# Kernel tuning notes

Hardware: AMD Instinct MI355X
Metric: run time of the kernel (lower is better)

## Reference

```python
import jax, jax.numpy as jnp
import numpy as np

DIM = 128; D_STATE = 16; D_CONV = 4; EXPAND = 2
D_INNER = DIM * EXPAND            # 256
DT_RANK = (DIM + 15) // 16        # 8
B, H, W = 2, 56, 56


def _ln(x, w, b):
    m = jnp.mean(x, -1, keepdims=True)
    v = jnp.var(x, -1, keepdims=True)
    return (x - m) * jax.lax.rsqrt(v + 1e-5) * w + b


def _mamba(x, in_w, conv_w, conv_b, xproj_w, dt_w, dt_b, A_log, Dp, out_w):
    # x: (B, L, DIM)
    Bb, L, _ = x.shape
    xz = x @ in_w.T                                   # (B,L,2*D_INNER)
    xi, z = jnp.split(xz, 2, axis=-1)
    # causal depthwise conv1d (pad left d_conv-1, truncate to L)
    xc = jnp.transpose(xi, (0, 2, 1))                 # (B,D_INNER,L)
    xc = jax.lax.conv_general_dilated(
        xc, conv_w, (1,), [(D_CONV - 1, 0)],
        dimension_numbers=('NCH', 'OIH', 'NCH'),
        feature_group_count=D_INNER) + conv_b[None, :, None]
    xs = jax.nn.silu(jnp.transpose(xc, (0, 2, 1)))    # (B,L,D_INNER)
    dbl = xs @ xproj_w.T                              # (B,L,DT_RANK+2*D_STATE)
    dt = jax.nn.softplus(dbl[..., :DT_RANK] @ dt_w.T + dt_b)   # (B,L,D_INNER)
    Bc = dbl[..., DT_RANK:DT_RANK + D_STATE]          # (B,L,D_STATE)
    Cc = dbl[..., DT_RANK + D_STATE:]                 # (B,L,D_STATE)
    A = -jnp.exp(A_log)                               # (D_INNER,D_STATE)
    dA = jnp.exp(dt[..., None] * A)                   # (B,L,D_INNER,D_STATE)
    dBu = (dt * xs)[..., None] * Bc[:, :, None, :]    # (B,L,D_INNER,D_STATE)

    def step(h, inp):
        a, bu, c = inp
        h = a * h + bu                                # (B,D_INNER,D_STATE)
        return h, jnp.einsum('bdn,bn->bd', h, c)

    h0 = jnp.zeros((Bb, D_INNER, D_STATE), x.dtype)
    _, ys = jax.lax.scan(step, h0, (jnp.moveaxis(dA, 1, 0),
                                    jnp.moveaxis(dBu, 1, 0),
                                    jnp.moveaxis(Cc, 1, 0)))
    y = jnp.moveaxis(ys, 0, 1) + xs * Dp              # (B,L,D_INNER)
    y = y * jax.nn.silu(z)
    return y @ out_w.T                                # (B,L,DIM)


def _forward(x, norm_h_w, norm_h_b, norm_v_w, norm_v_b,
             dw_w, dw_b, pw_w, pw_b,
             h_in_w, h_conv_w, h_conv_b, h_xproj_w, h_dt_w, h_dt_b, h_A_log, h_D, h_out_w,
             v_in_w, v_conv_w, v_conv_b, v_xproj_w, v_dt_w, v_dt_b, v_A_log, v_D, v_out_w,
             ca_fc1_w, ca_fc2_w):
    Bb, C, Hh, Ww = x.shape
    # local branch: depthwise 3x3 + GELU + 1x1
    lf = jax.lax.conv_general_dilated(
        x, dw_w, (1, 1), [(1, 1), (1, 1)],
        dimension_numbers=('NCHW', 'OIHW', 'NCHW'),
        feature_group_count=C) + dw_b[None, :, None, None]
    lf = jax.nn.gelu(lf, approximate=False)
    lf = jnp.einsum('bchw,oc->bohw', lf, pw_w[:, :, 0, 0]) + pw_b[None, :, None, None]
    # horizontal scan: row-major tokens
    xh = _ln(x.reshape(Bb, C, Hh * Ww).transpose(0, 2, 1), norm_h_w, norm_h_b)
    oh = _mamba(xh, h_in_w, h_conv_w, h_conv_b, h_xproj_w, h_dt_w, h_dt_b,
                h_A_log, h_D, h_out_w)
    oh = oh.transpose(0, 2, 1).reshape(Bb, C, Hh, Ww)
    # vertical scan: column-major tokens
    xv = _ln(jnp.transpose(x, (0, 1, 3, 2)).reshape(Bb, C, Ww * Hh).transpose(0, 2, 1),
             norm_v_w, norm_v_b)
    ov = _mamba(xv, v_in_w, v_conv_w, v_conv_b, v_xproj_w, v_dt_w, v_dt_b,
                v_A_log, v_D, v_out_w)
    ov = jnp.transpose(ov.transpose(0, 2, 1).reshape(Bb, C, Ww, Hh), (0, 1, 3, 2))
    fused = oh + ov + lf
    # channel attention
    y = jnp.mean(fused, axis=(2, 3))                  # (B,C)
    y = jax.nn.sigmoid(jax.nn.relu(y @ ca_fc1_w.T) @ ca_fc2_w.T)
    return fused * y[:, :, None, None] + x


def setup_inputs() -> dict:
    key = jax.random.key(0)
    ks = iter(jax.random.split(key, 64))
    def nrm(shape, scale):
        return jax.random.normal(next(ks), shape, jnp.float32) * scale
    d = {}
    d['x'] = nrm((B, DIM, H, W), 1.0)
    d['norm_h_w'] = jnp.ones((DIM,), jnp.float32); d['norm_h_b'] = jnp.zeros((DIM,), jnp.float32)
    d['norm_v_w'] = jnp.ones((DIM,), jnp.float32); d['norm_v_b'] = jnp.zeros((DIM,), jnp.float32)
    d['dw_w'] = nrm((DIM, 1, 3, 3), 1.0 / 3.0)
    d['dw_b'] = jnp.zeros((DIM,), jnp.float32)
    d['pw_w'] = nrm((DIM, DIM, 1, 1), DIM ** -0.5)
    d['pw_b'] = jnp.zeros((DIM,), jnp.float32)
    for p in ('h', 'v'):
        d[p + '_in_w'] = nrm((2 * D_INNER, DIM), DIM ** -0.5)
        d[p + '_conv_w'] = nrm((D_INNER, 1, D_CONV), D_CONV ** -0.5)
        d[p + '_conv_b'] = jnp.zeros((D_INNER,), jnp.float32)
        d[p + '_xproj_w'] = nrm((DT_RANK + 2 * D_STATE, D_INNER), D_INNER ** -0.5)
        d[p + '_dt_w'] = nrm((D_INNER, DT_RANK), DT_RANK ** -0.5)
        d[p + '_dt_b'] = jnp.full((D_INNER,), -2.0, jnp.float32)  # small positive dt
        d[p + '_A_log'] = jnp.log(jnp.tile(jnp.arange(1, D_STATE + 1, dtype=jnp.float32), (D_INNER, 1)))
        d[p + '_D'] = jnp.ones((D_INNER,), jnp.float32)
        d[p + '_out_w'] = nrm((DIM, D_INNER), D_INNER ** -0.5)
    d['ca_fc1_w'] = nrm((DIM // 4, DIM), DIM ** -0.5)
    d['ca_fc2_w'] = nrm((DIM, DIM // 4), (DIM // 4) ** -0.5)
    return d


def reference(x, norm_h_w, norm_h_b, norm_v_w, norm_v_b,
              dw_w, dw_b, pw_w, pw_b,
              h_in_w, h_conv_w, h_conv_b, h_xproj_w, h_dt_w, h_dt_b, h_A_log, h_D, h_out_w,
              v_in_w, v_conv_w, v_conv_b, v_xproj_w, v_dt_w, v_dt_b, v_A_log, v_D, v_out_w,
              ca_fc1_w, ca_fc2_w):
    return _forward(x, norm_h_w, norm_h_b, norm_v_w, norm_v_b,
                    dw_w, dw_b, pw_w, pw_b,
                    h_in_w, h_conv_w, h_conv_b, h_xproj_w, h_dt_w, h_dt_b, h_A_log, h_D, h_out_w,
                    v_in_w, v_conv_w, v_conv_b, v_xproj_w, v_dt_w, v_dt_b, v_A_log, v_D, v_out_w,
                    ca_fc1_w, ca_fc2_w)
```

## Files before the change

kernel.cpp:

```cpp
#include <hip/hip_runtime.h>
#include <hip/hip_bf16.h>

typedef __hip_bfloat16 bf16;
__device__ __forceinline__ float b2f(bf16 v){ return __bfloat162float(v); }
__device__ __forceinline__ bf16 f2b(float v){ return __float2bfloat16(v); }

typedef __attribute__((ext_vector_type(8))) short frag_ab;
typedef __attribute__((ext_vector_type(4))) float frag_cd;
typedef __attribute__((ext_vector_type(4))) short short4v;

__device__ __forceinline__ frag_ab ld_frag_2xb64(const bf16* p){
  union { frag_ab f; short4v h[2]; } u;
  u.h[0] = *reinterpret_cast<const short4v*>(p);
  u.h[1] = *reinterpret_cast<const short4v*>(p+4);
  return u.f;
}

__device__ __forceinline__ void st_agent(float* p, float v){
  __hip_atomic_store(p, v, __ATOMIC_RELAXED, __HIP_MEMORY_SCOPE_AGENT);
}
__device__ __forceinline__ float ld_agent(const float* p){
  return __hip_atomic_load(p, __ATOMIC_RELAXED, __HIP_MEMORY_SCOPE_AGENT);
}

#define LLEN 3136
#define BATCH 2
#define NCHUNK 49
#define LC 64

__global__ void k_front(const float* __restrict__ x, const float* __restrict__ dww,
                        const float* __restrict__ dwb, bf16* __restrict__ tmp,
                        const float* nhw_, const float* nhb_, const float* nvw_,
                        const float* nvb_, bf16* __restrict__ xln,
                        float* __restrict__ YMEAN, int* __restrict__ ZCNT,
                        const float* __restrict__ h_inw, const float* __restrict__ v_inw,
                        const float* __restrict__ h_ow,  const float* __restrict__ v_ow,
                        const float* __restrict__ pww,   const float* __restrict__ h_xw,
                        const float* __restrict__ v_xw,
                        bf16* __restrict__ WBIN, bf16* __restrict__ WBOUT,
                        bf16* __restrict__ WBPW, bf16* __restrict__ WBX){
  int blk = blockIdx.x;
  int tid = threadIdx.x;
  if (blk < 1024){
    int bc = blk & 255;
    int seg = blk >> 8;
    int c = bc & 127;
    if (blk == 0){
      if (tid < 256) YMEAN[tid] = 0.f;
      if (tid < 4)   ZCNT[tid] = 0;
    }
    const float* xp = x + (size_t)bc*LLEN;
    __shared__ float sxr[16][60];
    int r0 = seg*14;
    for (int idx = tid; idx < 16*56; idx += 256){
      int rr = idx/56, cc = idx%56;
      int gr = r0 - 1 + rr;
      sxr[rr][cc+1] = (gr >= 0 && gr < 56) ? xp[gr*56+cc] : 0.f;
    }
    if (tid < 16){ sxr[tid][0] = 0.f; sxr[tid][57] = 0.f; }
    float w[9];
    #pragma unroll
    for (int i=0;i<9;i++) w[i] = dww[c*9+i];
    float bias = dwb[c];
    __syncthreads();
    int pstart = seg * 784;
    for (int p = pstart + tid; p < pstart + 784; p += 256){
      int i = p/56, j = p%56;
      int li = i - r0;
      float acc = bias;
      #pragma unroll
      for (int a=0;a<3;a++)
        #pragma unroll
        for (int bb=0;bb<3;bb++)
          acc += w[a*3+bb] * sxr[li+a][j+bb];
      float g = 0.5f*acc*(1.0f + erff(acc*0.70710678118654752f));
      tmp[(size_t)bc*LLEN + p] = f2b(g);
    }
  } else if (blk < 1136){
    int idx2 = blk - 1024;
    int h = idx2 % 56, b = idx2 / 56;
    __shared__ float sx[128][57];
    __shared__ float smean[56], srstd[56];
    __shared__ float wh[128], bh[128], wv_[128], bv_[128];
    if (tid < 128){ wh[tid]=nhw_[tid]; bh[tid]=nhb_[tid];
                    wv_[tid]=nvw_[tid]; bv_[tid]=nvb_[tid]; }
    for (int idx = tid; idx < 128*56; idx += 256){
      int c = idx / 56, w = idx % 56;
      sx[c][w] = x[((size_t)(b*128+c))*LLEN + h*56 + w];
    }
    __syncthreads();
    if (tid < 56){
      float s=0.f, s2=0.f;
      for (int c=0;c<128;c++){ float v = sx[c][tid]; s+=v; s2+=v*v; }
      float m = s*(1.f/128.f);
      float var = s2*(1.f/128.f) - m*m;
      smean[tid]=m; srstd[tid]=rsqrtf(var+1e-5f);
    }
    __syncthreads();
    bf16* outh = xln;
    bf16* outv = xln + (size_t)BATCH*LLEN*128;
    for (int idx = tid; idx < 56*128; idx += 256){
      int w = idx >> 7, c = idx & 127;
      float v = (sx[c][w]-smean[w])*srstd[w];
      outh[((size_t)b*LLEN + h*56 + w)*128 + c] = f2b(v*wh[c]+bh[c]);
      outv[((size_t)b*LLEN + w*56 + h)*128 + c] = f2b(v*wv_[c]+bv_[c]);
    }
  } else {
    int pblk = blk - 1136;
    int t16 = tid*16;
    if (pblk < 32){
      int g = pblk*4096 + t16;
      int dir = g >> 16, off = g & 65535;
      const float* src = (dir ? v_inw : h_inw) + off;
      bf16* dst = WBIN + g;
      #pragma unroll
      for (int r=0;r<4;r++){
        float4 w4 = *reinterpret_cast<const float4*>(src + r*4);
        bf16 t4[4] = {f2b(w4.x), f2b(w4.y), f2b(w4.z), f2b(w4.w)};
        *reinterpret_cast<double*>(dst + r*4) = *reinterpret_cast<double*>(t4);
      }
    } else if (pblk < 48){
      int g = (pblk-32)*4096 + t16;
      int dir = g >> 15, off = g & 32767;
      const float* src = (dir ? v_ow : h_ow) + off;
      bf16* dst = WBOUT + g;
      #pragma unroll
      for (int r=0;r<4;r++){
        float4 w4 = *reinterpret_cast<const float4*>(src + r*4);
        bf16 t4[4] = {f2b(w4.x), f2b(w4.y), f2b(w4.z), f2b(w4.w)};
        *reinterpret_cast<double*>(dst + r*4) = *reinterpret_cast<double*>(t4);
      }
    } else if (pblk < 52){
      int g = (pblk-48)*4096 + t16;
      const float* src = pww + g;
      bf16* dst = WBPW + g;
      #pragma unroll
      for (int r=0;r<4;r++){
        float4 w4 = *reinterpret_cast<const float4*>(src + r*4);
        bf16 t4[4] = {f2b(w4.x), f2b(w4.y), f2b(w4.z), f2b(w4.w)};
        *reinterpret_cast<double*>(dst + r*4) = *reinterpret_cast<double*>(t4);
      }
    } else if (pblk < 58){
      int g = (pblk-52)*4096 + t16;
      int dir = (g >= 12288) ? 1 : 0;
      int off = g - dir*12288;
      int rr = off >> 8, cc = off & 255;
      bf16* dst = WBX + g;
      if (rr < 40){
        const float* src = (dir ? v_xw : h_xw) + rr*256 + cc;
        #pragma unroll
        for (int r=0;r<4;r++){
          float4 w4 = *reinterpret_cast<const float4*>(src + r*4);
          bf16 t4[4] = {f2b(w4.x), f2b(w4.y), f2b(w4.z), f2b(w4.w)};
          *reinterpret_cast<double*>(dst + r*4) = *reinterpret_cast<double*>(t4);
        }
      } else {
        bf16 z4[4] = {f2b(0.f), f2b(0.f), f2b(0.f), f2b(0.f)};
        double zd = *reinterpret_cast<double*>(z4);
        #pragma unroll
        for (int r=0;r<4;r++) *reinterpret_cast<double*>(dst + r*4) = zd;
      }
    }
  }
}

__global__ void k_inproj(const bf16* __restrict__ xln, const bf16* __restrict__ WBIN,
                         bf16* __restrict__ XI, bf16* __restrict__ Z){
  int dir = blockIdx.z;
  const bf16* A = xln + (size_t)dir*BATCH*LLEN*128;
  const bf16* Wb = WBIN + (size_t)dir*512*128;
  int m0 = blockIdx.x*64;
  int npair = blockIdx.y*128;
  __shared__ __align__(16) bf16 sA[64][136];
  __shared__ __align__(16) bf16 sW[64][136];
  int tid = threadIdx.x;
  #pragma unroll
  for (int r=0;r<4;r++){
    int idx = tid + r*256;
    int row = idx >> 4, c8 = (idx & 15)*8;
    *reinterpret_cast<float4*>(&sA[row][c8]) =
        *reinterpret_cast<const float4*>(&A[(size_t)(m0+row)*128 + c8]);
  }
  int wv2 = tid >> 6, lane = tid & 63;
  int qd = lane >> 4, mr = lane & 15;
  bf16* dst = (npair < 256) ? XI : Z;
  int nbase0 = npair & 255;
  size_t dslab = (size_t)dir*BATCH*LLEN*256;
  #pragma unroll
  for (int nt=0; nt<2; nt++){
    int n0 = npair + nt*64;
    __syncthreads();
    #pragma unroll
    for (int r=0;r<4;r++){
      int idx = tid + r*256;
      int row = idx >> 4, c8 = (idx & 15)*8;
      *reinterpret_cast<float4*>(&sW[row][c8]) =
          *reinterpret_cast<const float4*>(&Wb[(size_t)(n0+row)*128 + c8]);
    }
    __syncthreads();
    frag_cd acc[4] = {};
    #pragma unroll
    for (int k0=0;k0<128;k0+=32){
      frag_ab af = *reinterpret_cast<frag_ab*>(&sA[wv2*16+mr][k0+qd*8]);
      #pragma unroll
      for (int t=0;t<4;t++){
        frag_ab bfr = *reinterpret_cast<frag_ab*>(&sW[t*16+mr][k0+qd*8]);
        acc[t] = __builtin_amdgcn_mfma_f32_16x16x32_bf16(af, bfr, acc[t], 0, 0, 0);
      }
    }
    int nb = nbase0 + nt*64;
    #pragma unroll
    for (int t=0;t<4;t++)
      #pragma unroll
      for (int r=0;r<4;r++){
        int row = m0 + wv2*16 + qd*4 + r;
        int col = nb + t*16 + mr;
        dst[dslab + (size_t)row*256 + col] = f2b(acc[t][r]);
      }
  }
}

__global__ void k_dbl(const bf16* __restrict__ XI,
                      const float* hcw, const float* hcb, const float* vcw, const float* vcb,
                      const bf16* __restrict__ WBX,
                      const float* hdw, const float* vdw, const float* hdb, const float* vdb,
                      bf16* __restrict__ XS2, bf16* __restrict__ DT2,
                      float* __restrict__ Bf, float* __restrict__ Cf){
  int m0 = blockIdx.x*64;
  int bd = m0 / LLEN;
  int l0m = m0 % LLEN;
  int dirq = bd >> 1;
  const bf16* XId = XI + (size_t)bd*LLEN*256;
  const bf16* Wb = WBX + (size_t)dirq*48*256;
  const float* cw = dirq ? vcw : hcw;
  const float* cb = dirq ? vcb : hcb;
  __shared__ __align__(16) bf16 sA[67][264];
  __shared__ __align__(16) bf16 sW[48][264];
  __shared__ float sdbl[64][49];
  int tid = threadIdx.x;
  for (int idx = tid; idx < 67*32; idx += 256){
    int row = idx >> 5, c8 = (idx & 31)*8;
    int l = l0m - 3 + row;
    float4 v = make_float4(0.f,0.f,0.f,0.f);
    if (l >= 0) v = *reinterpret_cast<const float4*>(&XId[(size_t)l*256 + c8]);
    *reinterpret_cast<float4*>(&sA[row][c8]) = v;
  }
  #pragma unroll
  for (int r=0;r<6;r++){
    int idx = tid + r*256;
    int row = idx >> 5, c8 = (idx & 31)*8;
    *reinterpret_cast<float4*>(&sW[row][c8]) =
        *reinterpret_cast<const float4*>(&Wb[(size_t)row*256 + c8]);
  }
  __syncthreads();
  {
    float w0=cw[tid*4], w1=cw[tid*4+1], w2=cw[tid*4+2], w3=cw[tid*4+3];
    float cbias = cb[tid];
    size_t x2base = ((size_t)bd*16 + (tid>>4))*LLEN + l0m;
    int c16 = tid & 15;
    float xm3 = b2f(sA[0][tid]), xm2 = b2f(sA[1][tid]), xm1 = b2f(sA[2][tid]);
    #pragma unroll 4
    for (int j=0;j<64;j++){
      float x0 = b2f(sA[j+3][tid]);
      float acc = cbias + w0*xm3 + w1*xm2 + w2*xm1 + w3*x0;
      float s = acc / (1.f + __expf(-acc));
      bf16 sv = f2b(s);
      sA[j][tid] = sv;
      XS2[(x2base + j)*16 + c16] = sv;
      xm3=xm2; xm2=xm1; xm1=x0;
    }
  }
  __syncthreads();
  int wv2 = tid >> 6, lane = tid & 63;
  int qd = lane >> 4, mr = lane & 15;
  frag_cd acc[3] = {};
  #pragma unroll
  for (int k0=0;k0<256;k0+=32){
    frag_ab af = *reinterpret_cast<frag_ab*>(&sA[wv2*16+mr][k0+qd*8]);
    #pragma unroll
    for (int t=0;t<3;t++){
      frag_ab bfr = *reinterpret_cast<frag_ab*>(&sW[t*16+mr][k0+qd*8]);
      acc[t] = __builtin_amdgcn_mfma_f32_16x16x32_bf16(af, bfr, acc[t], 0, 0, 0);
    }
  }
  #pragma unroll
  for (int t=0;t<3;t++)
    #pragma unroll
    for (int r=0;r<4;r++){
      int col = t*16 + mr;
      if (col < 40) sdbl[wv2*16 + qd*4 + r][col] = acc[t][r];
    }
  __syncthreads();
  const float* dtw = dirq ? vdw : hdw;
  const float* dtb = dirq ? vdb : hdb;
  float w8[8];
  #pragma unroll
  for (int r=0;r<8;r++) w8[r] = dtw[tid*8+r];
  float biasv = dtb[tid];
  size_t d2base = ((size_t)bd*16 + (tid>>4))*LLEN + l0m;
  int c16 = tid & 15;
  for (int row=0; row<64; row++){
    float a = biasv;
    #pragma unroll
    for (int r=0;r<8;r++) a += sdbl[row][r]*w8[r];
    float sv = (a > 20.f) ? a : __logf(1.f + __expf(a));
    DT2[(d2base + row)*16 + c16] = f2b(sv);
  }
  #pragma unroll
  for (int r=0;r<8;r++){
    int idx = tid + r*256;
    int row = idx >> 5, o = idx & 31;
    float v = sdbl[row][8+o];
    size_t rr = (size_t)(m0+row)*16;
    if (o < 16) Bf[rr + o] = v;
    else        Cf[rr + (o-16)] = v;
  }
}

__global__ void k_scan1(const bf16* __restrict__ DT2, const bf16* __restrict__ XS2,
                        const float* __restrict__ Bc, const float* hA, const float* vA,
                        float* __restrict__ Pbuf, float* __restrict__ Hbuf){
  int bd = blockIdx.z;
  int g  = blockIdx.y;
  int ck = blockIdx.x;
  int l0 = ck*LC;
  const float* Bd = Bc + (size_t)bd*LLEN*16;
  const float* Alog = (bd >> 1) ? vA : hA;
  int tid = threadIdx.x;
  int dl = tid >> 4, n = tid & 15;
  float A = -__expf(Alog[(g*16+dl)*16+n]);
  __shared__ float sdt[LC][16], sxs[LC][16], sB[LC][16];
  size_t base2 = (((size_t)bd*16 + g)*LLEN + l0)*16;
  #pragma unroll
  for (int r=0;r<4;r++){
    int idx = tid + r*256;
    sdt[idx>>4][idx&15] = b2f(DT2[base2 + idx]);
    sxs[idx>>4][idx&15] = b2f(XS2[base2 + idx]);
    (&sB[0][0])[idx] = Bd[(size_t)l0*16 + idx];
  }
  __syncthreads();
  float h = 0.f, P = 1.f;
  #pragma unroll 8
  for (int i=0;i<LC;i++){
    float a = sdt[i][dl];
    float u = sxs[i][dl];
    float dA = __expf(a * A);
    h = dA*h + (a*u)*sB[i][n];
    P *= dA;
  }
  size_t sidx = (((size_t)bd*16 + g)*NCHUNK + ck)*256 + tid;
  Pbuf[sidx] = P;
  Hbuf[sidx] = h;
}

__global__ void k_scan2(const float* __restrict__ Pbuf, float* __restrict__ Hbuf){
  int q = blockIdx.x;
  int tid = threadIdx.x;
  size_t qb = (size_t)q*NCHUNK*256 + tid;
  float Pv[7], Hv[7];
  float carry = 0.f;
  #pragma unroll
  for (int j=0;j<7;j++){
    Pv[j] = Pbuf[qb + (size_t)j*256];
    Hv[j] = Hbuf[qb + (size_t)j*256];
  }
  #pragma unroll
  for (int b=0;b<7;b++){
    float Pn[7], Hn[7];
    if (b < 6){
      #pragma unroll
      for (int j=0;j<7;j++){
        Pn[j] = Pbuf[qb + (size_t)((b+1)*7+j)*256];
        Hn[j] = Hbuf[qb + (size_t)((b+1)*7+j)*256];
      }
    }
    #pragma unroll
    for (int j=0;j<7;j++){
      Hbuf[qb + (size_t)(b*7+j)*256] = carry;
      carry = Pv[j]*carry + Hv[j];
    }
    if (b < 6){
      #pragma unroll
      for (int j=0;j<7;j++){ Pv[j] = Pn[j]; Hv[j] = Hn[j]; }
    }
  }
}

__global__ void k_scan3(const bf16* __restrict__ DT2, const bf16* __restrict__ XS2,
                        const float* __restrict__ Bc, const float* __restrict__ Cc,
                        const float* hA, const float* vA,
                        const float* __restrict__ Hbuf, bf16* __restrict__ ys){
  int bd = blockIdx.z;
  int g  = blockIdx.y;
  int ck = blockIdx.x;
  int l0 = ck*LC;
  const float* Bd = Bc + (size_t)bd*LLEN*16;
  const float* Cd = Cc + (size_t)bd*LLEN*16;
  bf16* yd = ys + (size_t)bd*LLEN*256;
  const float* Alog = (bd >> 1) ? vA : hA;
  int tid = threadIdx.x;
  int dl = tid >> 4, n = tid & 15;
  float A = -__expf(Alog[(g*16+dl)*16+n]);
  __shared__ float sdt[LC][16], sxs[LC][16], sB[LC][16], sC[LC][16];
  __shared__ float sp2[16][272];
  size_t base2 = (((size_t)bd*16 + g)*LLEN + l0)*16;
  #pragma unroll
  for (int r=0;r<4;r++){
    int idx = tid + r*256;
    sdt[idx>>4][idx&15] = b2f(DT2[base2 + idx]);
    sxs[idx>>4][idx&15] = b2f(XS2[base2 + idx]);
    (&sB[0][0])[idx] = Bd[(size_t)l0*16 + idx];
    (&sC[0][0])[idx] = Cd[(size_t)l0*16 + idx];
  }
  size_t sidx = (((size_t)bd*16 + g)*NCHUNK + ck)*256 + tid;
  float h = Hbuf[sidx];
  __syncthreads();
  int swz = dl*17 + n;
  int i_local = tid >> 4;
  int c16 = tid & 15;
  int rbase = c16*17;
  for (int i0=0; i0<LC; i0+=16){
    #pragma unroll
    for (int ii=0;ii<16;ii++){
      int i = i0 + ii;
      float a = sdt[i][dl];
      float u = sxs[i][dl];
      float dA = __expf(a * A);
      h = dA*h + (a*u)*sB[i][n];
      sp2[ii][swz] = h * sC[i][n];
    }
    __syncthreads();
    const float* row = &sp2[i_local][rbase];
    float s = 0.f;
    #pragma unroll
    for (int k=0;k<16;k++) s += row[k];
    yd[(size_t)(l0+i0+i_local)*256 + g*16 + c16] = f2b(s);
    __syncthreads();
  }
}

__global__ void k_outgemm(const bf16* __restrict__ ys, const bf16* __restrict__ XS2,
                          const bf16* __restrict__ Z, const float* __restrict__ hD,
                          const float* __restrict__ vD, const bf16* __restrict__ WBOUT,
                          bf16* __restrict__ OD){
  int dir = blockIdx.y;
  size_t slab = (size_t)dir*BATCH*LLEN*256;
  const bf16* Wb = WBOUT + (size_t)dir*128*256;
  const float* Dw = dir ? vD : hD;
  bf16* od = OD + (size_t)dir*BATCH*LLEN*128;
  int m0 = blockIdx.x*32;
  int bd = dir*2 + m0/LLEN;
  int lbase = m0 % LLEN;
  __shared__ __align__(16) bf16 sA[32][264];
  __shared__ __align__(16) bf16 sW[64][264];
  int tid = threadIdx.x;
  #pragma unroll
  for (int r=0;r<4;r++){
    int idx = tid + r*256;
    int row = idx >> 5, c8 = (idx & 31)*8;
    size_t e = slab + (size_t)(m0+row)*256 + c8;
    size_t e2 = (((size_t)bd*16 + (c8>>4))*LLEN + lbase + row)*16 + (c8&15);
    bf16 yb[8], xb[8], zb[8], ob[8];
    *reinterpret_cast<float4*>(yb) = *reinterpret_cast<const float4*>(&ys[e]);
    *reinterpret_cast<float4*>(xb) = *reinterpret_cast<const float4*>(&XS2[e2]);
    *reinterpret_cast<float4*>(zb) = *reinterpret_cast<const float4*>(&Z[e]);
    #pragma unroll
    for (int j=0;j<8;j++){
      float Dv = Dw[c8 + j];
      float yv = b2f(yb[j]) + b2f(xb[j])*Dv;
      float zv = b2f(zb[j]);
      ob[j] = f2b(yv * (zv/(1.f+__expf(-zv))));
    }
    *reinterpret_cast<float4*>(&sA[row][c8]) = *reinterpret_cast<float4*>(ob);
  }
  int wv2 = tid >> 6, lane = tid & 63;
  int qd = lane >> 4, mr = lane & 15;
  int msub = wv2 & 1, tpair = (wv2 >> 1)*2;
  #pragma unroll
  for (int nh=0; nh<2; nh++){
    int n0 = nh*64;
    __syncthreads();
    #pragma unroll
    for (int r=0;r<8;r++){
      int idx = tid + r*256;
      int row = idx >> 5, c8 = (idx & 31)*8;
      *reinterpret_cast<float4*>(&sW[row][c8]) =
          *reinterpret_cast<const float4*>(&Wb[(size_t)(n0+row)*256 + c8]);
    }
    __syncthreads();
    frag_cd acc[2] = {};
    #pragma unroll
    for (int k0=0;k0<256;k0+=32){
      frag_ab af = *reinterpret_cast<frag_ab*>(&sA[msub*16+mr][k0+qd*8]);
      #pragma unroll
      for (int i=0;i<2;i++){
        frag_ab bfr = *reinterpret_cast<frag_ab*>(&sW[(tpair+i)*16+mr][k0+qd*8]);
        acc[i] = __builtin_amdgcn_mfma_f32_16x16x32_bf16(af, bfr, acc[i], 0, 0, 0);
      }
    }
    #pragma unroll
    for (int i=0;i<2;i++)
      #pragma unroll
      for (int r=0;r<4;r++){
        int row = m0 + msub*16 + qd*4 + r;
        int col = n0 + (tpair+i)*16 + mr;
        od[(size_t)row*128 + col] = f2b(acc[i][r]);
      }
  }
}

__global__ void k_pwcomb(const bf16* __restrict__ tmp, const bf16* __restrict__ WBPW,
                         const float* __restrict__ pwb, const bf16* __restrict__ OD,
                         const float* __restrict__ x, float* __restrict__ out,
                         float* __restrict__ YMEAN, int* __restrict__ CNTPW,
                         int* __restrict__ FLAG, float* __restrict__ GATE,
                         const float* __restrict__ fc1, const float* __restrict__ fc2){
  int p0 = blockIdx.x * 64;
  int m0 = blockIdx.y * 64;
  int b  = blockIdx.z;
  const bf16* T = tmp + (size_t)b*128*LLEN;
  const bf16* od0 = OD + (size_t)b*LLEN*128;
  const bf16* od1 = OD + (size_t)(BATCH + b)*LLEN*128;
  __shared__ __align__(16) bf16 sA[64][136];
  __shared__ __align__(16) bf16 sBt[64][132];
  __shared__ float sOD[64][65];
  __shared__ float ym[128], s1g[32];
  __shared__ int slast;
  int tid = threadIdx.x;
  #pragma unroll
  for (int r=0;r<4;r++){
    int idx = tid + r*256;
    int row = idx >> 4, c8 = (idx & 15)*8;
    *reinterpret_cast<float4*>(&sA[row][c8]) =
        *reinterpret_cast<const float4*>(&WBPW[(size_t)(m0+row)*128 + c8]);
  }
  #pragma unroll
  for (int r=0;r<8;r++){
    int idx = tid + r*256;
    int c = idx >> 4, p4 = (idx & 15)*4;
    union { double d; bf16 v[4]; } u;
    u.d = *reinterpret_cast<const double*>(&T[(size_t)c*LLEN + p0 + p4]);
    #pragma unroll
    for (int j=0;j<4;j++) sBt[p4+j][c] = u.v[j];
  }
  #pragma unroll
  for (int r=0;r<8;r++){
    int idx = tid + r*256;
    int prow = idx >> 5, mp = (idx & 31)*2;
    int p = p0 + prow;
    int pi = p/56, pj = p%56;
    int pt = pj*56 + pi;
    bf16 a0[2], a1[2];
    *reinterpret_cast<float*>(a0) = *reinterpret_cast<const float*>(&od0[(size_t)p*128 + m0 + mp]);
    *reinterpret_cast<float*>(a1) = *reinterpret_cast<const float*>(&od1[(size_t)pt*128 + m0 + mp]);
    sOD[prow][mp]   = b2f(a0[0]) + b2f(a1[0]);
    sOD[prow][mp+1] = b2f(a0[1]) + b2f(a1[1]);
  }
  __syncthreads();
  int wv2 = tid >> 6, lane = tid & 63;
  int qd = lane >> 4, mr = lane & 15;
  frag_cd acc[4] = {};
  #pragma unroll
  for (int k0=0;k0<128;k0+=32){
    frag_ab af = *reinterpret_cast<frag_ab*>(&sA[wv2*16+mr][k0+qd*8]);
    #pragma unroll
    for (int t=0;t<4;t++){
      frag_ab bfr = ld_frag_2xb64(&sBt[t*16+mr][k0+qd*8]);
      acc[t] = __builtin_amdgcn_mfma_f32_16x16x32_bf16(af, bfr, acc[t], 0, 0, 0);
    }
  }
  float vals[4][4];
  #pragma unroll
  for (int r=0;r<4;r++){
    int m = m0 + wv2*16 + qd*4 + r;
    float bias = pwb[m];
    float s = 0.f;
    #pragma unroll
    for (int t=0;t<4;t++){
      float val = acc[t][r] + bias + sOD[t*16+mr][m - m0];
      vals[t][r] = val;
      s += val;
    }
    s += __shfl_xor(s, 1, 16);
    s += __shfl_xor(s, 2, 16);
    s += __shfl_xor(s, 4, 16);
    s += __shfl_xor(s, 8, 16);
    if (mr == 0) atomicAdd(&YMEAN[b*128 + m], s);
  }
  __syncthreads();
  if (tid == 0) slast = (atomicAdd(&CNTPW[b], 1) == 2*49 - 1);
  __syncthreads();
  if (slast){
    if (tid < 128)
      ym[tid] = ld_agent(&YMEAN[b*128+tid]) * (1.f/(float)LLEN);
    __syncthreads();
    {
      int o = tid >> 3, part = tid & 7;
      float a = 0.f;
      #pragma unroll
      for (int k=0;k<16;k++) a += ym[part*16 + k] * fc1[o*128 + part*16 + k];
      a += __shfl_xor(a, 1, 8);
      a += __shfl_xor(a, 2, 8);
      a += __shfl_xor(a, 4, 8);
      if (part == 0) s1g[o] = fmaxf(a, 0.f);
    }
    __syncthreads();
    if (tid < 128){
      float a = 0.f;
      #pragma unroll
      for (int j=0;j<32;j++) a += s1g[j]*fc2[tid*32+j];
      st_agent(&GATE[b*128+tid], 1.f/(1.f+__expf(-a)));
    }
    __syncthreads();
    if (tid == 0)
      __hip_atomic_store(&FLAG[b], 1, __ATOMIC_RELEASE, __HIP_MEMORY_SCOPE_AGENT);
  } else {
    if (tid == 0)
      while (__hip_atomic_load(&FLAG[b], __ATOMIC_ACQUIRE, __HIP_MEMORY_SCOPE_AGENT) == 0)
        __builtin_amdgcn_s_sleep(2);
  }
  __syncthreads();
  float g4[4];
  #pragma unroll
  for (int r=0;r<4;r++){
    int m = m0 + wv2*16 + qd*4 + r;
    g4[r] = ld_agent(&GATE[b*128+m]);
  }
  #pragma unroll
  for (int t=0;t<4;t++)
    #pragma unroll
    for (int r=0;r<4;r++){
      int m = m0 + wv2*16 + qd*4 + r;
      int p = p0 + t*16 + mr;
      size_t i = ((size_t)b*128 + m)*LLEN + p;
      out[i] = vals[t][r]*g4[r] + x[i];
    }
}

extern "C" void kernel_launch(void* const* d_in, const int* in_sizes, int n_in,
                              void* d_out, int out_size, void* d_ws, size_t ws_size,
                              hipStream_t stream) {
  const float* x      = (const float*)d_in[0];
  const float* nhw    = (const float*)d_in[1];
  const float* nhb    = (const float*)d_in[2];
  const float* nvw    = (const float*)d_in[3];
  const float* nvb    = (const float*)d_in[4];
  const float* dww    = (const float*)d_in[5];
  const float* dwb    = (const float*)d_in[6];
  const float* pww    = (const float*)d_in[7];
  const float* pwb    = (const float*)d_in[8];
  const float* h_inw  = (const float*)d_in[9];
  const float* h_cw   = (const float*)d_in[10];
  const float* h_cb   = (const float*)d_in[11];
  const float* h_xw   = (const float*)d_in[12];
  const float* h_dtw  = (const float*)d_in[13];
  const float* h_dtb  = (const float*)d_in[14];
  const float* h_Al   = (const float*)d_in[15];
  const float* h_D    = (const float*)d_in[16];
  const float* h_ow   = (const float*)d_in[17];
  const float* v_inw  = (const float*)d_in[18];
  const float* v_cw   = (const float*)d_in[19];
  const float* v_cb   = (const float*)d_in[20];
  const float* v_xw   = (const float*)d_in[21];
  const float* v_dtw  = (const float*)d_in[22];
  const float* v_dtb  = (const float*)d_in[23];
  const float* v_Al   = (const float*)d_in[24];
  const float* v_D    = (const float*)d_in[25];
  const float* v_ow   = (const float*)d_in[26];
  const float* fc1    = (const float*)d_in[27];
  const float* fc2    = (const float*)d_in[28];

  float* out = (float*)d_out;

  bf16* WBIN  = (bf16*)((char*)d_out + 0);
  bf16* WBOUT = (bf16*)((char*)d_out + 262144);
  bf16* WBX   = (bf16*)((char*)d_out + 393216);

  char* base = (char*)d_ws;
  bf16*  XLN   = (bf16*)(base + 1605632);
  bf16*  DT2   = (bf16*)(base + 0);
  bf16*  OD    = (bf16*)(base + 0);
  bf16*  XI    = (bf16*)(base + 6422528);
  bf16*  YS    = (bf16*)(base + 6422528);
  bf16*  Z     = (bf16*)(base + 12845056);
  bf16*  XS2   = (bf16*)(base + 19267584);
  float* Bf    = (float*)(base + 25690112);
  float* Cf    = (float*)(base + 26492928);
  float* Hbuf  = (float*)(base + 27295744);
  float* YMEAN = (float*)(base + 30507008);
  bf16*  TMP   = (bf16*)(base + 30508032);
  float* Pbuf  = (float*)(base + 32113664);
  int*   ZCNT  = (int*)  (base + 35324928);
  float* GATE  = (float*)(base + 35325440);
  bf16*  WBPW  = (bf16*) (base + 35326464);
  int*   CNTPW = ZCNT;
  int*   FLAG  = ZCNT + 2;

  k_front<<<dim3(1024 + 56*BATCH + 64), dim3(256), 0, stream>>>(
      x, dww, dwb, TMP, nhw, nhb, nvw, nvb, XLN, YMEAN, ZCNT,
      h_inw, v_inw, h_ow, v_ow, pww, h_xw, v_xw, WBIN, WBOUT, WBPW, WBX);
  k_inproj<<<dim3(98,4,2), dim3(256), 0, stream>>>(XLN, WBIN, XI, Z);
  k_dbl<<<dim3(196), dim3(256), 0, stream>>>(XI, h_cw, h_cb, v_cw, v_cb,
                                             WBX, h_dtw, v_dtw, h_dtb, v_dtb,
                                             XS2, DT2, Bf, Cf);
  k_scan1<<<dim3(NCHUNK,16,4), dim3(256), 0, stream>>>(DT2, XS2, Bf, h_Al, v_Al, Pbuf, Hbuf);
  k_scan2<<<dim3(64), dim3(256), 0, stream>>>(Pbuf, Hbuf);
  k_scan3<<<dim3(NCHUNK,16,4), dim3(256), 0, stream>>>(DT2, XS2, Bf, Cf, h_Al, v_Al, Hbuf, YS);
  k_outgemm<<<dim3(196,2), dim3(256), 0, stream>>>(YS, XS2, Z, h_D, v_D, WBOUT, OD);
  k_pwcomb<<<dim3(49,2,BATCH), dim3(256), 0, stream>>>(TMP, WBPW, pwb, OD, x, out,
                                                       YMEAN, CNTPW, FLAG, GATE, fc1, fc2);
}
```

Measured before the change: 220.4 us.

## Fuse chunk-local scan into k_dbl and fold carry propagation into k_scan3

Computes each chunk's local scan state and decay product directly inside k_dbl, with each thread handling one channel across all 16 states. This removes the k_scan1 and k_scan2 launches and the re-read of DT/XS/B. k_scan3 now rebuilds its incoming carry by serially combining all preceding chunk summaries. The cost is extra serial exp work per k_dbl thread and redundant carry recomputation in later chunks, which grows with the chunk index.

```diff
diff --git a/kernel.cpp b/kernel.cpp
--- a/kernel.cpp
+++ b/kernel.cpp
@@ -224,8 +224,10 @@
                       const float* hcw, const float* hcb, const float* vcw, const float* vcb,
                       const bf16* __restrict__ WBX,
                       const float* hdw, const float* vdw, const float* hdb, const float* vdb,
+                      const float* hA, const float* vA,
                       bf16* __restrict__ XS2, bf16* __restrict__ DT2,
-                      float* __restrict__ Bf, float* __restrict__ Cf){
+                      float* __restrict__ Bf, float* __restrict__ Cf,
+                      float* __restrict__ Pbuf, float* __restrict__ Hbuf){
   int m0 = blockIdx.x*64;
   int bd = m0 / LLEN;
   int l0m = m0 % LLEN;
@@ -297,6 +299,21 @@
   #pragma unroll
   for (int r=0;r<8;r++) w8[r] = dtw[tid*8+r];
   float biasv = dtb[tid];
+  float A16[16];
+  {
+    const float* Alog = dirq ? vA : hA;
+    #pragma unroll
+    for (int n4=0;n4<4;n4++){
+      float4 al = *reinterpret_cast<const float4*>(&Alog[tid*16 + n4*4]);
+      A16[n4*4+0] = -__expf(al.x);
+      A16[n4*4+1] = -__expf(al.y);
+      A16[n4*4+2] = -__expf(al.z);
+      A16[n4*4+3] = -__expf(al.w);
+    }
+  }
+  float hs[16], Ps[16];
+  #pragma unroll
+  for (int n=0;n<16;n++){ hs[n]=0.f; Ps[n]=1.f; }
   size_t d2base = ((size_t)bd*16 + (tid>>4))*LLEN + l0m;
   int c16 = tid & 15;
   for (int row=0; row<64; row++){
@@ -304,7 +321,28 @@
     #pragma unroll
     for (int r=0;r<8;r++) a += sdbl[row][r]*w8[r];
     float sv = (a > 20.f) ? a : __logf(1.f + __expf(a));
-    DT2[(d2base + row)*16 + c16] = f2b(sv);
+    bf16 dtb16 = f2b(sv);
+    DT2[(d2base + row)*16 + c16] = dtb16;
+    float av = b2f(dtb16);
+    float u  = b2f(sA[row][tid]);
+    float au = av*u;
+    #pragma unroll
+    for (int n=0;n<16;n++){
+      float Bv = sdbl[row][8+n];
+      float dA = __expf(av * A16[n]);
+      hs[n] = dA*hs[n] + au*Bv;
+      Ps[n] *= dA;
+    }
+  }
+  {
+    size_t pbase = (((size_t)bd*16 + (tid>>4))*NCHUNK + (size_t)(l0m>>6))*256 + (size_t)c16*16;
+    #pragma unroll
+    for (int n4=0;n4<4;n4++){
+      *reinterpret_cast<float4*>(&Pbuf[pbase + n4*4]) =
+          make_float4(Ps[n4*4], Ps[n4*4+1], Ps[n4*4+2], Ps[n4*4+3]);
+      *reinterpret_cast<float4*>(&Hbuf[pbase + n4*4]) =
+          make_float4(hs[n4*4], hs[n4*4+1], hs[n4*4+2], hs[n4*4+3]);
+    }
   }
   #pragma unroll
   for (int r=0;r<8;r++){
@@ -317,79 +355,11 @@
   }
 }
 
-__global__ void k_scan1(const bf16* __restrict__ DT2, const bf16* __restrict__ XS2,
-                        const float* __restrict__ Bc, const float* hA, const float* vA,
-                        float* __restrict__ Pbuf, float* __restrict__ Hbuf){
-  int bd = blockIdx.z;
-  int g  = blockIdx.y;
-  int ck = blockIdx.x;
-  int l0 = ck*LC;
-  const float* Bd = Bc + (size_t)bd*LLEN*16;
-  const float* Alog = (bd >> 1) ? vA : hA;
-  int tid = threadIdx.x;
-  int dl = tid >> 4, n = tid & 15;
-  float A = -__expf(Alog[(g*16+dl)*16+n]);
-  __shared__ float sdt[LC][16], sxs[LC][16], sB[LC][16];
-  size_t base2 = (((size_t)bd*16 + g)*LLEN + l0)*16;
-  #pragma unroll
-  for (int r=0;r<4;r++){
-    int idx = tid + r*256;
-    sdt[idx>>4][idx&15] = b2f(DT2[base2 + idx]);
-    sxs[idx>>4][idx&15] = b2f(XS2[base2 + idx]);
-    (&sB[0][0])[idx] = Bd[(size_t)l0*16 + idx];
-  }
-  __syncthreads();
-  float h = 0.f, P = 1.f;
-  #pragma unroll 8
-  for (int i=0;i<LC;i++){
-    float a = sdt[i][dl];
-    float u = sxs[i][dl];
-    float dA = __expf(a * A);
-    h = dA*h + (a*u)*sB[i][n];
-    P *= dA;
-  }
-  size_t sidx = (((size_t)bd*16 + g)*NCHUNK + ck)*256 + tid;
-  Pbuf[sidx] = P;
-  Hbuf[sidx] = h;
-}
-
-__global__ void k_scan2(const float* __restrict__ Pbuf, float* __restrict__ Hbuf){
-  int q = blockIdx.x;
-  int tid = threadIdx.x;
-  size_t qb = (size_t)q*NCHUNK*256 + tid;
-  float Pv[7], Hv[7];
-  float carry = 0.f;
-  #pragma unroll
-  for (int j=0;j<7;j++){
-    Pv[j] = Pbuf[qb + (size_t)j*256];
-    Hv[j] = Hbuf[qb + (size_t)j*256];
-  }
-  #pragma unroll
-  for (int b=0;b<7;b++){
-    float Pn[7], Hn[7];
-    if (b < 6){
-      #pragma unroll
-      for (int j=0;j<7;j++){
-        Pn[j] = Pbuf[qb + (size_t)((b+1)*7+j)*256];
-        Hn[j] = Hbuf[qb + (size_t)((b+1)*7+j)*256];
-      }
-    }
-    #pragma unroll
-    for (int j=0;j<7;j++){
-      Hbuf[qb + (size_t)(b*7+j)*256] = carry;
-      carry = Pv[j]*carry + Hv[j];
-    }
-    if (b < 6){
-      #pragma unroll
-      for (int j=0;j<7;j++){ Pv[j] = Pn[j]; Hv[j] = Hn[j]; }
-    }
-  }
-}
-
 __global__ void k_scan3(const bf16* __restrict__ DT2, const bf16* __restrict__ XS2,
                         const float* __restrict__ Bc, const float* __restrict__ Cc,
                         const float* hA, const float* vA,
-                        const float* __restrict__ Hbuf, bf16* __restrict__ ys){
+                        const float* __restrict__ Pbuf, const float* __restrict__ Hbuf,
+                        bf16* __restrict__ ys){
   int bd = blockIdx.z;
   int g  = blockIdx.y;
   int ck = blockIdx.x;
@@ -412,8 +382,23 @@
     (&sB[0][0])[idx] = Bd[(size_t)l0*16 + idx];
     (&sC[0][0])[idx] = Cd[(size_t)l0*16 + idx];
   }
-  size_t sidx = (((size_t)bd*16 + g)*NCHUNK + ck)*256 + tid;
-  float h = Hbuf[sidx];
+  float h = 0.f;
+  {
+    size_t qbase = (size_t)(bd*16 + g)*NCHUNK*256 + tid;
+    int k = 0;
+    for (; k+8 <= ck; k += 8){
+      float Pv[8], Hv[8];
+      #pragma unroll
+      for (int j=0;j<8;j++){
+        Pv[j] = Pbuf[qbase + (size_t)(k+j)*256];
+        Hv[j] = Hbuf[qbase + (size_t)(k+j)*256];
+      }
+      #pragma unroll
+      for (int j=0;j<8;j++) h = Pv[j]*h + Hv[j];
+    }
+    for (; k < ck; ++k)
+      h = Pbuf[qbase + (size_t)k*256]*h + Hbuf[qbase + (size_t)k*256];
+  }
   __syncthreads();
   int swz = dl*17 + n;
   int i_local = tid >> 4;
@@ -702,10 +687,10 @@
   k_inproj<<<dim3(98,4,2), dim3(256), 0, stream>>>(XLN, WBIN, XI, Z);
   k_dbl<<<dim3(196), dim3(256), 0, stream>>>(XI, h_cw, h_cb, v_cw, v_cb,
                                              WBX, h_dtw, v_dtw, h_dtb, v_dtb,
-                                             XS2, DT2, Bf, Cf);
-  k_scan1<<<dim3(NCHUNK,16,4), dim3(256), 0, stream>>>(DT2, XS2, Bf, h_Al, v_Al, Pbuf, Hbuf);
-  k_scan2<<<dim3(64), dim3(256), 0, stream>>>(Pbuf, Hbuf);
-  k_scan3<<<dim3(NCHUNK,16,4), dim3(256), 0, stream>>>(DT2, XS2, Bf, Cf, h_Al, v_Al, Hbuf, YS);
+                                             h_Al, v_Al,
+                                             XS2, DT2, Bf, Cf, Pbuf, Hbuf);
+  k_scan3<<<dim3(NCHUNK,16,4), dim3(256), 0, stream>>>(DT2, XS2, Bf, Cf, h_Al, v_Al,
+                                                       Pbuf, Hbuf, YS);
   k_outgemm<<<dim3(196,2), dim3(256), 0, stream>>>(YS, XS2, Z, h_D, v_D, WBOUT, OD);
   k_pwcomb<<<dim3(49,2,BATCH), dim3(256), 0, stream>>>(TMP, WBPW, pwb, OD, x, out,
                                                        YMEAN, CNTPW, FLAG, GATE, fc1, fc2);
```

Result: slower. 227.6 us (+3.3%).

## Split GEMM kernels into more blocks and double k_dbl threads

Applied to the files above, without the earlier changes.

k_inproj and k_outgemm now give each block a single 64-column N tile instead of looping over two, which doubles the grid. k_pwcomb halves its spatial tile to 32 positions and doubles its block count, with the last-block counter threshold updated to match. k_dbl runs with 512 threads, and each half computes the conv/SiLU and dt softplus for 32 of the 64 rows; the second half holds its first three outputs in registers until after a barrier so it does not overwrite inputs the first half still reads. The aim is more parallelism on a small problem. In exchange, k_outgemm blocks redo the A-tile load (including the D and gating elementwise work), and k_pwcomb has more blocks spin-waiting on the global flag.

```diff
diff --git a/kernel.cpp b/kernel.cpp
--- a/kernel.cpp
+++ b/kernel.cpp
@@ -170,7 +170,7 @@
   const bf16* A = xln + (size_t)dir*BATCH*LLEN*128;
   const bf16* Wb = WBIN + (size_t)dir*512*128;
   int m0 = blockIdx.x*64;
-  int npair = blockIdx.y*128;
+  int n0 = blockIdx.y*64;
   __shared__ __align__(16) bf16 sA[64][136];
   __shared__ __align__(16) bf16 sW[64][136];
   int tid = threadIdx.x;
@@ -180,44 +180,33 @@
     int row = idx >> 4, c8 = (idx & 15)*8;
     *reinterpret_cast<float4*>(&sA[row][c8]) =
         *reinterpret_cast<const float4*>(&A[(size_t)(m0+row)*128 + c8]);
-  }
+    *reinterpret_cast<float4*>(&sW[row][c8]) =
+        *reinterpret_cast<const float4*>(&Wb[(size_t)(n0+row)*128 + c8]);
+  }
+  __syncthreads();
   int wv2 = tid >> 6, lane = tid & 63;
   int qd = lane >> 4, mr = lane & 15;
-  bf16* dst = (npair < 256) ? XI : Z;
-  int nbase0 = npair & 255;
+  bf16* dst = (n0 < 256) ? XI : Z;
+  int nb = n0 & 255;
   size_t dslab = (size_t)dir*BATCH*LLEN*256;
-  #pragma unroll
-  for (int nt=0; nt<2; nt++){
-    int n0 = npair + nt*64;
-    __syncthreads();
+  frag_cd acc[4] = {};
+  #pragma unroll
+  for (int k0=0;k0<128;k0+=32){
+    frag_ab af = *reinterpret_cast<frag_ab*>(&sA[wv2*16+mr][k0+qd*8]);
+    #pragma unroll
+    for (int t=0;t<4;t++){
+      frag_ab bfr = *reinterpret_cast<frag_ab*>(&sW[t*16+mr][k0+qd*8]);
+      acc[t] = __builtin_amdgcn_mfma_f32_16x16x32_bf16(af, bfr, acc[t], 0, 0, 0);
+    }
+  }
+  #pragma unroll
+  for (int t=0;t<4;t++)
     #pragma unroll
     for (int r=0;r<4;r++){
-      int idx = tid + r*256;
-      int row = idx >> 4, c8 = (idx & 15)*8;
-      *reinterpret_cast<float4*>(&sW[row][c8]) =
-          *reinterpret_cast<const float4*>(&Wb[(size_t)(n0+row)*128 + c8]);
-    }
-    __syncthreads();
-    frag_cd acc[4] = {};
-    #pragma unroll
-    for (int k0=0;k0<128;k0+=32){
-      frag_ab af = *reinterpret_cast<frag_ab*>(&sA[wv2*16+mr][k0+qd*8]);
-      #pragma unroll
-      for (int t=0;t<4;t++){
-        frag_ab bfr = *reinterpret_cast<frag_ab*>(&sW[t*16+mr][k0+qd*8]);
-        acc[t] = __builtin_amdgcn_mfma_f32_16x16x32_bf16(af, bfr, acc[t], 0, 0, 0);
-      }
-    }
-    int nb = nbase0 + nt*64;
-    #pragma unroll
-    for (int t=0;t<4;t++)
-      #pragma unroll
-      for (int r=0;r<4;r++){
-        int row = m0 + wv2*16 + qd*4 + r;
-        int col = nb + t*16 + mr;
-        dst[dslab + (size_t)row*256 + col] = f2b(acc[t][r]);
-      }
-  }
+      int row = m0 + wv2*16 + qd*4 + r;
+      int col = nb + t*16 + mr;
+      dst[dslab + (size_t)row*256 + col] = f2b(acc[t][r]);
+    }
 }
 
 __global__ void k_dbl(const bf16* __restrict__ XI,
@@ -238,7 +227,7 @@
   __shared__ __align__(16) bf16 sW[48][264];
   __shared__ float sdbl[64][49];
   int tid = threadIdx.x;
-  for (int idx = tid; idx < 67*32; idx += 256){
+  for (int idx = tid; idx < 67*32; idx += 512){
     int row = idx >> 5, c8 = (idx & 31)*8;
     int l = l0m - 3 + row;
     float4 v = make_float4(0.f,0.f,0.f,0.f);
@@ -246,69 +235,88 @@
     *reinterpret_cast<float4*>(&sA[row][c8]) = v;
   }
   #pragma unroll
-  for (int r=0;r<6;r++){
-    int idx = tid + r*256;
+  for (int r=0;r<3;r++){
+    int idx = tid + r*512;
     int row = idx >> 5, c8 = (idx & 31)*8;
     *reinterpret_cast<float4*>(&sW[row][c8]) =
         *reinterpret_cast<const float4*>(&Wb[(size_t)row*256 + c8]);
   }
   __syncthreads();
   {
-    float w0=cw[tid*4], w1=cw[tid*4+1], w2=cw[tid*4+2], w3=cw[tid*4+3];
-    float cbias = cb[tid];
-    size_t x2base = ((size_t)bd*16 + (tid>>4))*LLEN + l0m;
-    int c16 = tid & 15;
-    float xm3 = b2f(sA[0][tid]), xm2 = b2f(sA[1][tid]), xm1 = b2f(sA[2][tid]);
-    #pragma unroll 4
-    for (int j=0;j<64;j++){
-      float x0 = b2f(sA[j+3][tid]);
+    int c = tid & 255;
+    int half = tid >> 8;
+    int j0 = half << 5;
+    float w0=cw[c*4], w1=cw[c*4+1], w2=cw[c*4+2], w3=cw[c*4+3];
+    float cbias = cb[c];
+    size_t x2base = ((size_t)bd*16 + (c>>4))*LLEN + l0m + j0;
+    int c16 = c & 15;
+    float xm3 = b2f(sA[j0][c]), xm2 = b2f(sA[j0+1][c]), xm1 = b2f(sA[j0+2][c]);
+    bf16 d0, d1, d2;
+    #pragma unroll
+    for (int jj=0;jj<32;jj++){
+      float x0 = b2f(sA[j0+jj+3][c]);
       float acc = cbias + w0*xm3 + w1*xm2 + w2*xm1 + w3*x0;
       float s = acc / (1.f + __expf(-acc));
       bf16 sv = f2b(s);
-      sA[j][tid] = sv;
-      XS2[(x2base + j)*16 + c16] = sv;
+      if (half){
+        if (jj==0) d0=sv; else if (jj==1) d1=sv; else if (jj==2) d2=sv;
+        else sA[j0+jj][c] = sv;
+      } else {
+        sA[j0+jj][c] = sv;
+      }
+      XS2[(x2base + jj)*16 + c16] = sv;
       xm3=xm2; xm2=xm1; xm1=x0;
     }
-  }
-  __syncthreads();
-  int wv2 = tid >> 6, lane = tid & 63;
-  int qd = lane >> 4, mr = lane & 15;
-  frag_cd acc[3] = {};
-  #pragma unroll
-  for (int k0=0;k0<256;k0+=32){
-    frag_ab af = *reinterpret_cast<frag_ab*>(&sA[wv2*16+mr][k0+qd*8]);
-    #pragma unroll
-    for (int t=0;t<3;t++){
-      frag_ab bfr = *reinterpret_cast<frag_ab*>(&sW[t*16+mr][k0+qd*8]);
-      acc[t] = __builtin_amdgcn_mfma_f32_16x16x32_bf16(af, bfr, acc[t], 0, 0, 0);
-    }
-  }
-  #pragma unroll
-  for (int t=0;t<3;t++)
-    #pragma unroll
-    for (int r=0;r<4;r++){
-      int col = t*16 + mr;
-      if (col < 40) sdbl[wv2*16 + qd*4 + r][col] = acc[t][r];
-    }
-  __syncthreads();
-  const float* dtw = dirq ? vdw : hdw;
-  const float* dtb = dirq ? vdb : hdb;
-  float w8[8];
-  #pragma unroll
-  for (int r=0;r<8;r++) w8[r] = dtw[tid*8+r];
-  float biasv = dtb[tid];
-  size_t d2base = ((size_t)bd*16 + (tid>>4))*LLEN + l0m;
-  int c16 = tid & 15;
-  for (int row=0; row<64; row++){
-    float a = biasv;
-    #pragma unroll
-    for (int r=0;r<8;r++) a += sdbl[row][r]*w8[r];
-    float sv = (a > 20.f) ? a : __logf(1.f + __expf(a));
-    DT2[(d2base + row)*16 + c16] = f2b(sv);
-  }
-  #pragma unroll
-  for (int r=0;r<8;r++){
-    int idx = tid + r*256;
+    __syncthreads();
+    if (half){ sA[j0][c]=d0; sA[j0+1][c]=d1; sA[j0+2][c]=d2; }
+  }
+  __syncthreads();
+  if (tid < 256){
+    int wv2 = tid >> 6, lane = tid & 63;
+    int qd = lane >> 4, mr = lane & 15;
+    frag_cd acc[3] = {};
+    #pragma unroll
+    for (int k0=0;k0<256;k0+=32){
+      frag_ab af = *reinterpret_cast<frag_ab*>(&sA[wv2*16+mr][k0+qd*8]);
+      #pragma unroll
+      for (int t=0;t<3;t++){
+        frag_ab bfr = *reinterpret_cast<frag_ab*>(&sW[t*16+mr][k0+qd*8]);
+        acc[t] = __builtin_amdgcn_mfma_f32_16x16x32_bf16(af, bfr, acc[t], 0, 0, 0);
+      }
+    }
+    #pragma unroll
+    for (int t=0;t<3;t++)
+      #pragma unroll
+      for (int r=0;r<4;r++){
+        int col = t*16 + mr;
+        if (col < 40) sdbl[wv2*16 + qd*4 + r][col] = acc[t][r];
+      }
+  }
+  __syncthreads();
+  {
+    const float* dtw = dirq ? vdw : hdw;
+    const float* dtb = dirq ? vdb : hdb;
+    int c = tid & 255;
+    int half = tid >> 8;
+    int j0 = half << 5;
+    float w8[8];
+    #pragma unroll
+    for (int r=0;r<8;r++) w8[r] = dtw[c*8+r];
+    float biasv = dtb[c];
+    size_t d2base = ((size_t)bd*16 + (c>>4))*LLEN + l0m + j0;
+    int c16 = c & 15;
+    for (int rr=0; rr<32; rr++){
+      int row = j0 + rr;
+      float a = biasv;
+      #pragma unroll
+      for (int r=0;r<8;r++) a += sdbl[row][r]*w8[r];
+      float sv = (a > 20.f) ? a : __logf(1.f + __expf(a));
+      DT2[(d2base + rr)*16 + c16] = f2b(sv);
+    }
+  }
+  #pragma unroll
+  for (int r=0;r<4;r++){
+    int idx = tid + r*512;
     int row = idx >> 5, o = idx & 31;
     float v = sdbl[row][8+o];
     size_t rr = (size_t)(m0+row)*16;
@@ -444,6 +452,7 @@
                           const float* __restrict__ vD, const bf16* __restrict__ WBOUT,
                           bf16* __restrict__ OD){
   int dir = blockIdx.y;
+  int n0 = blockIdx.z*64;
   size_t slab = (size_t)dir*BATCH*LLEN*256;
   const bf16* Wb = WBOUT + (size_t)dir*128*256;
   const float* Dw = dir ? vD : hD;
@@ -473,40 +482,35 @@
     }
     *reinterpret_cast<float4*>(&sA[row][c8]) = *reinterpret_cast<float4*>(ob);
   }
+  #pragma unroll
+  for (int r=0;r<8;r++){
+    int idx = tid + r*256;
+    int row = idx >> 5, c8 = (idx & 31)*8;
+    *reinterpret_cast<float4*>(&sW[row][c8]) =
+        *reinterpret_cast<const float4*>(&Wb[(size_t)(n0+row)*256 + c8]);
+  }
+  __syncthreads();
   int wv2 = tid >> 6, lane = tid & 63;
   int qd = lane >> 4, mr = lane & 15;
   int msub = wv2 & 1, tpair = (wv2 >> 1)*2;
-  #pragma unroll
-  for (int nh=0; nh<2; nh++){
-    int n0 = nh*64;
-    __syncthreads();
-    #pragma unroll
-    for (int r=0;r<8;r++){
-      int idx = tid + r*256;
-      int row = idx >> 5, c8 = (idx & 31)*8;
-      *reinterpret_cast<float4*>(&sW[row][c8]) =
-          *reinterpret_cast<const float4*>(&Wb[(size_t)(n0+row)*256 + c8]);
-    }
-    __syncthreads();
-    frag_cd acc[2] = {};
-    #pragma unroll
-    for (int k0=0;k0<256;k0+=32){
-      frag_ab af = *reinterpret_cast<frag_ab*>(&sA[msub*16+mr][k0+qd*8]);
-      #pragma unroll
-      for (int i=0;i<2;i++){
-        frag_ab bfr = *reinterpret_cast<frag_ab*>(&sW[(tpair+i)*16+mr][k0+qd*8]);
-        acc[i] = __builtin_amdgcn_mfma_f32_16x16x32_bf16(af, bfr, acc[i], 0, 0, 0);
-      }
-    }
-    #pragma unroll
-    for (int i=0;i<2;i++)
-      #pragma unroll
-      for (int r=0;r<4;r++){
-        int row = m0 + msub*16 + qd*4 + r;
-        int col = n0 + (tpair+i)*16 + mr;
-        od[(size_t)row*128 + col] = f2b(acc[i][r]);
-      }
-  }
+  frag_cd acc[2] = {};
+  #pragma unroll
+  for (int k0=0;k0<256;k0+=32){
+    frag_ab af = *reinterpret_cast<frag_ab*>(&sA[msub*16+mr][k0+qd*8]);
+    #pragma unroll
+    for (int i=0;i<2;i++){
+      frag_ab bfr = *reinterpret_cast<frag_ab*>(&sW[(tpair+i)*16+mr][k0+qd*8]);
+      acc[i] = __builtin_amdgcn_mfma_f32_16x16x32_bf16(af, bfr, acc[i], 0, 0, 0);
+    }
+  }
+  #pragma unroll
+  for (int i=0;i<2;i++)
+    #pragma unroll
+    for (int r=0;r<4;r++){
+      int row = m0 + msub*16 + qd*4 + r;
+      int col = n0 + (tpair+i)*16 + mr;
+      od[(size_t)row*128 + col] = f2b(acc[i][r]);
+    }
 }
 
 __global__ void k_pwcomb(const bf16* __restrict__ tmp, const bf16* __restrict__ WBPW,
@@ -515,15 +519,15 @@
                          float* __restrict__ YMEAN, int* __restrict__ CNTPW,
                          int* __restrict__ FLAG, float* __restrict__ GATE,
                          const float* __restrict__ fc1, const float* __restrict__ fc2){
-  int p0 = blockIdx.x * 64;
+  int p0 = blockIdx.x * 32;
   int m0 = blockIdx.y * 64;
   int b  = blockIdx.z;
   const bf16* T = tmp + (size_t)b*128*LLEN;
   const bf16* od0 = OD + (size_t)b*LLEN*128;
   const bf16* od1 = OD + (size_t)(BATCH + b)*LLEN*128;
   __shared__ __align__(16) bf16 sA[64][136];
-  __shared__ __align__(16) bf16 sBt[64][132];
-  __shared__ float sOD[64][65];
+  __shared__ __align__(16) bf16 sBt[32][132];
+  __shared__ float sOD[32][65];
   __shared__ float ym[128], s1g[32];
   __shared__ int slast;
   int tid = threadIdx.x;
@@ -535,16 +539,16 @@
         *reinterpret_cast<const float4*>(&WBPW[(size_t)(m0+row)*128 + c8]);
   }
   #pragma unroll
-  for (int r=0;r<8;r++){
+  for (int r=0;r<4;r++){
     int idx = tid + r*256;
-    int c = idx >> 4, p4 = (idx & 15)*4;
+    int c = idx >> 3, p4 = (idx & 7)*4;
     union { double d; bf16 v[4]; } u;
     u.d = *reinterpret_cast<const double*>(&T[(size_t)c*LLEN + p0 + p4]);
     #pragma unroll
     for (int j=0;j<4;j++) sBt[p4+j][c] = u.v[j];
   }
   #pragma unroll
-  for (int r=0;r<8;r++){
+  for (int r=0;r<4;r++){
     int idx = tid + r*256;
     int prow = idx >> 5, mp = (idx & 31)*2;
     int p = p0 + prow;
@@ -559,24 +563,24 @@
   __syncthreads();
   int wv2 = tid >> 6, lane = tid & 63;
   int qd = lane >> 4, mr = lane & 15;
-  frag_cd acc[4] = {};
+  frag_cd acc[2] = {};
   #pragma unroll
   for (int k0=0;k0<128;k0+=32){
     frag_ab af = *reinterpret_cast<frag_ab*>(&sA[wv2*16+mr][k0+qd*8]);
     #pragma unroll
-    for (int t=0;t<4;t++){
+    for (int t=0;t<2;t++){
       frag_ab bfr = ld_frag_2xb64(&sBt[t*16+mr][k0+qd*8]);
       acc[t] = __builtin_amdgcn_mfma_f32_16x16x32_bf16(af, bfr, acc[t], 0, 0, 0);
     }
   }
-  float vals[4][4];
+  float vals[2][4];
   #pragma unroll
   for (int r=0;r<4;r++){
     int m = m0 + wv2*16 + qd*4 + r;
     float bias = pwb[m];
     float s = 0.f;
     #pragma unroll
-    for (int t=0;t<4;t++){
+    for (int t=0;t<2;t++){
       float val = acc[t][r] + bias + sOD[t*16+mr][m - m0];
       vals[t][r] = val;
       s += val;
@@ -588,7 +592,7 @@
     if (mr == 0) atomicAdd(&YMEAN[b*128 + m], s);
   }
   __syncthreads();
-  if (tid == 0) slast = (atomicAdd(&CNTPW[b], 1) == 2*49 - 1);
+  if (tid == 0) slast = (atomicAdd(&CNTPW[b], 1) == 2*98 - 1);
   __syncthreads();
   if (slast){
     if (tid < 128)
@@ -627,7 +631,7 @@
     g4[r] = ld_agent(&GATE[b*128+m]);
   }
   #pragma unroll
-  for (int t=0;t<4;t++)
+  for (int t=0;t<2;t++)
     #pragma unroll
     for (int r=0;r<4;r++){
       int m = m0 + wv2*16 + qd*4 + r;
@@ -699,14 +703,14 @@
   k_front<<<dim3(1024 + 56*BATCH + 64), dim3(256), 0, stream>>>(
       x, dww, dwb, TMP, nhw, nhb, nvw, nvb, XLN, YMEAN, ZCNT,
       h_inw, v_inw, h_ow, v_ow, pww, h_xw, v_xw, WBIN, WBOUT, WBPW, WBX);
-  k_inproj<<<dim3(98,4,2), dim3(256), 0, stream>>>(XLN, WBIN, XI, Z);
-  k_dbl<<<dim3(196), dim3(256), 0, stream>>>(XI, h_cw, h_cb, v_cw, v_cb,
+  k_inproj<<<dim3(98,8,2), dim3(256), 0, stream>>>(XLN, WBIN, XI, Z);
+  k_dbl<<<dim3(196), dim3(512), 0, stream>>>(XI, h_cw, h_cb, v_cw, v_cb,
                                              WBX, h_dtw, v_dtw, h_dtb, v_dtb,
                                              XS2, DT2, Bf, Cf);
   k_scan1<<<dim3(NCHUNK,16,4), dim3(256), 0, stream>>>(DT2, XS2, Bf, h_Al, v_Al, Pbuf, Hbuf);
   k_scan2<<<dim3(64), dim3(256), 0, stream>>>(Pbuf, Hbuf);
   k_scan3<<<dim3(NCHUNK,16,4), dim3(256), 0, stream>>>(DT2, XS2, Bf, Cf, h_Al, v_Al, Hbuf, YS);
-  k_outgemm<<<dim3(196,2), dim3(256), 0, stream>>>(YS, XS2, Z, h_D, v_D, WBOUT, OD);
-  k_pwcomb<<<dim3(49,2,BATCH), dim3(256), 0, stream>>>(TMP, WBPW, pwb, OD, x, out,
+  k_outgemm<<<dim3(196,2,2), dim3(256), 0, stream>>>(YS, XS2, Z, h_D, v_D, WBOUT, OD);
+  k_pwcomb<<<dim3(98,2,BATCH), dim3(256), 0, stream>>>(TMP, WBPW, pwb, OD, x, out,
                                                        YMEAN, CNTPW, FLAG, GATE, fc1, fc2);
 }
```

Result: slower. 235.5 us (+6.8%).
